# Kernel tuning notes

Measured on AMD Instinct MI355X. Metric: run time of the kernel, lower is better.

The kernel has to match this reference:

```python
import jax, jax.numpy as jnp
import numpy as np

B = 256      # number of graphs (args.batch_size)
NPG = 1000   # nodes per graph (args.num_node)
C = 64       # in_channels
DEG = 16     # avg degree
K = 500      # ceil(ratio * NPG), ratio = 0.5
EPS = 1e-8


def setup_inputs() -> dict:
    key = jax.random.key(0)
    k1, k2, k3, k4, k5 = jax.random.split(key, 5)
    N = B * NPG
    epg = NPG * DEG  # edges per graph
    x = jax.random.normal(k1, (N, C), jnp.float32)
    src = jax.random.randint(k2, (B, epg), 0, NPG)
    dst = jax.random.randint(k3, (B, epg), 0, NPG)
    off = (jnp.arange(B, dtype=jnp.int32) * NPG)[:, None]
    edge_index = jnp.stack([(src + off).reshape(-1), (dst + off).reshape(-1)]).astype(jnp.int32)
    edge_attr = jax.random.uniform(k4, (B * epg,), jnp.float32)
    batch = jnp.repeat(jnp.arange(B, dtype=jnp.int32), NPG)
    W = jax.random.normal(k5, (C, C), jnp.float32) * (1.0 / np.sqrt(C))
    b = jnp.zeros((C,), jnp.float32)
    return {"istraining": 1, "x": x, "edge_index": edge_index, "edge_attr": edge_attr,
            "batch": batch, "W": W, "b": b}


def _gcn_conv(x, edge_index, W, b):
    # PyG GCNConv: x' = D^{-1/2} (A + I) D^{-1/2} X W + b, unit edge weights.
    N = x.shape[0]
    sl = jnp.arange(N, dtype=edge_index.dtype)
    src = jnp.concatenate([edge_index[0], sl])  # message source j
    dst = jnp.concatenate([edge_index[1], sl])  # aggregation target i
    deg = jnp.zeros((N,), x.dtype).at[dst].add(1.0)
    dinv = jnp.where(deg > 0, jax.lax.rsqrt(jnp.maximum(deg, 1.0)), 0.0)
    norm = dinv[src] * dinv[dst]          # [E+N]
    h = x @ W                              # [N, C]
    msg = h[src] * norm[:, None]           # gather + scale (dominant traffic)
    out = jax.ops.segment_sum(msg, dst, num_segments=N) + b
    return out


def _node_score(x):
    # compute_node_score: cosine similarity of each node to its graph centroid
    # (community prototype), plus KL(softmax(score) || uniform) per graph.
    xb = x.reshape(B, NPG, C)
    cen = xb.mean(axis=1, keepdims=True)                       # [B,1,C]
    num = jnp.sum(xb * cen, axis=-1)                           # [B,NPG]
    den = jnp.linalg.norm(xb, axis=-1) * jnp.linalg.norm(cen, axis=-1) + EPS
    score = num / den                                          # [B,NPG]
    logp = jax.nn.log_softmax(score, axis=1)
    kl = jnp.sum(jnp.exp(logp) * (logp + jnp.log(jnp.float32(NPG))), axis=1)  # [B]
    indices_ = jnp.argsort(-score, axis=1)                     # [B,NPG]
    return score, kl, indices_


def reference(istraining, x, edge_index, edge_attr, batch, W, b):
    N = x.shape[0]
    x = _gcn_conv(x, edge_index, W, b)
    score, kl_all_batch, indices_ = _node_score(x)
    # per-graph top-k (fixed k since every graph has NPG nodes)
    _, idx = jax.lax.top_k(score, K)                           # [B,K]
    perm = ((jnp.arange(B, dtype=idx.dtype) * NPG)[:, None] + idx).reshape(-1)  # [B*K]
    score_flat = score.reshape(-1)
    x_new = x[perm] * jnp.tanh(score_flat[perm])[:, None]
    batch_new = batch[perm]
    # filter_adj: keep edges with both endpoints retained, re-index to new ids.
    mapping = jnp.full((N,), -1, dtype=jnp.int32).at[perm].set(
        jnp.arange(perm.shape[0], dtype=jnp.int32))
    new_ei = mapping[edge_index]                               # [2,E], -1 = dropped
    edge_mask = jnp.logical_and(new_ei[0] >= 0, new_ei[1] >= 0)
    edge_attr_new = jnp.where(edge_mask, edge_attr, 0.0)
    return (x_new, new_ei, edge_attr_new, edge_mask, batch_new, perm, kl_all_batch, indices_)
```

## Files before the change

kernel.cpp:

```cpp
#include <hip/hip_runtime.h>
#include <math.h>

#define NPG 1000
#define KTOP 500
#define C 64
#define EPG 16000
#define BPG 63

__device__ __forceinline__ float readlane_f(float v, int l) {
    return __uint_as_float(__builtin_amdgcn_readlane(__float_as_uint(v), (unsigned)l));
}
__device__ __forceinline__ int readlane_i(int v, int l) {
    return (int)__builtin_amdgcn_readlane((unsigned)v, (unsigned)l);
}

__global__ __launch_bounds__(1024) void build_graph_k(const int* __restrict__ ei, int E,
                                                      int* __restrict__ deg,
                                                      float* __restrict__ dinv,
                                                      int* __restrict__ off,
                                                      int* __restrict__ csr) {
    int g = blockIdx.x, t = threadIdx.x;
    __shared__ int cnt[NPG];
    __shared__ int soff[NPG];
    __shared__ unsigned short lcsr[EPG];
    __shared__ int red[1024];
    const int gbase = g * NPG;
    const int ebase = g * EPG;
    const int* __restrict__ srcp = ei + ebase;
    const int* __restrict__ dstp = ei + E + ebase;

    for (int i = t; i < NPG; i += 1024) cnt[i] = 0;
    __syncthreads();
    for (int i = t; i < EPG; i += 1024) atomicAdd(&cnt[dstp[i] - gbase], 1);
    __syncthreads();
    int v = (t < NPG) ? cnt[t] : 0;
    red[t] = v;
    __syncthreads();
    for (int o = 1; o < 1024; o <<= 1) {
        int xx = (t >= o) ? red[t - o] : 0;
        __syncthreads();
        red[t] += xx;
        __syncthreads();
    }
    if (t < NPG) soff[t] = red[t] - v;
    __syncthreads();
    for (int i = t; i < NPG; i += 1024) {
        int d = cnt[i];
        deg[gbase + i] = d;
        dinv[gbase + i] = 1.0f / sqrtf((float)(d + 1));
        off[gbase + i] = ebase + soff[i];
    }
    __syncthreads();
    for (int i = t; i < NPG; i += 1024) cnt[i] = soff[i];
    __syncthreads();
    for (int i = t; i < EPG; i += 1024) {
        int d = dstp[i] - gbase;
        int pos = atomicAdd(&cnt[d], 1);
        lcsr[pos] = (unsigned short)(srcp[i] - gbase);
    }
    __syncthreads();
    int4* co = (int4*)(csr + ebase);
    for (int i = t; i < EPG / 4; i += 1024) {
        int4 vv;
        vv.x = gbase + (int)lcsr[i * 4 + 0];
        vv.y = gbase + (int)lcsr[i * 4 + 1];
        vv.z = gbase + (int)lcsr[i * 4 + 2];
        vv.w = gbase + (int)lcsr[i * 4 + 3];
        co[i] = vv;
    }
}

__global__ __launch_bounds__(256) void gemm_k(const float* __restrict__ x,
                                              const float* __restrict__ W,
                                              const float* __restrict__ dinv,
                                              float* __restrict__ h2, int N) {
    __shared__ float sW[C * C];
    int t = threadIdx.x;
    for (int i = t; i < C * C / 4; i += 256) ((float4*)sW)[i] = ((const float4*)W)[i];
    __syncthreads();
    int r0 = blockIdx.x * 512 + t;
    int r1 = r0 + 256;
    if (r0 >= N) return;
    bool has1 = (r1 < N);
    const float4* x0 = (const float4*)(x + (size_t)r0 * C);
    const float4* x1 = (const float4*)(x + (size_t)(has1 ? r1 : r0) * C);
    float acc0[C], acc1[C];
#pragma unroll
    for (int i = 0; i < C; ++i) { acc0[i] = 0.f; acc1[i] = 0.f; }
    float4 a0 = x0[0], a1 = x1[0];
    for (int k4 = 0; k4 < 16; ++k4) {
        float4 b0, b1;
        if (k4 < 15) { b0 = x0[k4 + 1]; b1 = x1[k4 + 1]; }
        const float4* wr = (const float4*)(sW + k4 * 4 * C);
        const float* a0f = (const float*)&a0;
        const float* a1f = (const float*)&a1;
#pragma unroll
        for (int c4 = 0; c4 < 16; ++c4) {
            float4 w[4];
            w[0] = wr[c4]; w[1] = wr[16 + c4]; w[2] = wr[32 + c4]; w[3] = wr[48 + c4];
            const float* wf = (const float*)w;
#pragma unroll
            for (int j = 0; j < 4; ++j) {
                float s0 = acc0[c4 * 4 + j], s1 = acc1[c4 * 4 + j];
#pragma unroll
                for (int kk = 0; kk < 4; ++kk) {
                    float wv = wf[kk * 4 + j];
                    s0 = fmaf(a0f[kk], wv, s0);
                    s1 = fmaf(a1f[kk], wv, s1);
                }
                acc0[c4 * 4 + j] = s0; acc1[c4 * 4 + j] = s1;
            }
        }
        a0 = b0; a1 = b1;
    }
    float dv0 = dinv[r0];
    float dv1 = has1 ? dinv[r1] : 0.f;
#pragma unroll
    for (int i = 0; i < C; ++i) { acc0[i] *= dv0; acc1[i] *= dv1; }
    float4* h0 = (float4*)(h2 + (size_t)r0 * C);
#pragma unroll
    for (int q = 0; q < 16; ++q) h0[q] = ((float4*)acc0)[q];
    if (has1) {
        float4* h1 = (float4*)(h2 + (size_t)r1 * C);
#pragma unroll
        for (int q = 0; q < 16; ++q) h1[q] = ((float4*)acc1)[q];
    }
}

__global__ __launch_bounds__(256) void gather_k(const int* __restrict__ csr,
                                                const int* __restrict__ off,
                                                const int* __restrict__ deg,
                                                const float* __restrict__ h2,
                                                const float* __restrict__ dinv,
                                                const float* __restrict__ bias,
                                                float* __restrict__ out2,
                                                float* __restrict__ cen_sum,
                                                int N, int B) {
    __shared__ float cenacc[C];
    int blk = blockIdx.x;
    int wave = threadIdx.x >> 6;
    int lane = threadIdx.x & 63;
    int t = threadIdx.x;
    int g, blkin;
    if ((B & 7) == 0) {
        int xcd = blk & 7, slot = blk >> 3;
        g = (slot / BPG) * 8 + xcd;
        blkin = slot % BPG;
    } else {
        g = blk / BPG;
        blkin = blk % BPG;
    }
    if (t < C) cenacc[t] = 0.f;
    __syncthreads();

    int base = blkin * 4 + wave;
    bool active = (base < NPG / 4);
    float csum = 0.f;
    if (active) {
        int nA = g * NPG + base;
        int nB = nA + 250, nC = nA + 500, nD = nA + 750;
        int oA = off[nA], oB = off[nB], oC = off[nC], oD = off[nD];
        int dA = deg[nA], dB = deg[nB], dC = deg[nC], dD = deg[nD];
        float diA = dinv[nA], diB = dinv[nB], diC = dinv[nC], diD = dinv[nD];
        float hA = h2[(size_t)nA * C + lane];
        float hB = h2[(size_t)nB * C + lane];
        float hC = h2[(size_t)nC * C + lane];
        float hD = h2[(size_t)nD * C + lane];
        float bv = bias[lane];
        int svA = (lane < dA) ? csr[oA + lane] : nA;
        int svB = (lane < dB) ? csr[oB + lane] : nB;
        int svC = (lane < dC) ? csr[oC + lane] : nC;
        int svD = (lane < dD) ? csr[oD + lane] : nD;
        int jmA = dA < 64 ? dA : 64;
        int jmB = dB < 64 ? dB : 64;
        int jmC = dC < 64 ? dC : 64;
        int jmD = dD < 64 ? dD : 64;
        int rA = (jmA + 3) & ~3, rB = (jmB + 3) & ~3;
        int rC = (jmC + 3) & ~3, rD = (jmD + 3) & ~3;
        int m0 = rA > rB ? rA : rB;
        int m1 = rC > rD ? rC : rD;
        int mmax = m0 > m1 ? m0 : m1;
        float aA = 0.f, aB = 0.f, aC = 0.f, aD = 0.f;
        for (int j = 0; j < mmax; j += 4) {
            int sA0 = readlane_i(svA, j + 0), sA1 = readlane_i(svA, j + 1);
            int sA2 = readlane_i(svA, j + 2), sA3 = readlane_i(svA, j + 3);
            int sB0 = readlane_i(svB, j + 0), sB1 = readlane_i(svB, j + 1);
            int sB2 = readlane_i(svB, j + 2), sB3 = readlane_i(svB, j + 3);
            int sC0 = readlane_i(svC, j + 0), sC1 = readlane_i(svC, j + 1);
            int sC2 = readlane_i(svC, j + 2), sC3 = readlane_i(svC, j + 3);
            int sD0 = readlane_i(svD, j + 0), sD1 = readlane_i(svD, j + 1);
            int sD2 = readlane_i(svD, j + 2), sD3 = readlane_i(svD, j + 3);
            float vA0 = h2[(size_t)sA0 * C + lane];
            float vA1 = h2[(size_t)sA1 * C + lane];
            float vA2 = h2[(size_t)sA2 * C + lane];
            float vA3 = h2[(size_t)sA3 * C + lane];
            float vB0 = h2[(size_t)sB0 * C + lane];
            float vB1 = h2[(size_t)sB1 * C + lane];
            float vB2 = h2[(size_t)sB2 * C + lane];
            float vB3 = h2[(size_t)sB3 * C + lane];
            float vC0 = h2[(size_t)sC0 * C + lane];
            float vC1 = h2[(size_t)sC1 * C + lane];
            float vC2 = h2[(size_t)sC2 * C + lane];
            float vC3 = h2[(size_t)sC3 * C + lane];
            float vD0 = h2[(size_t)sD0 * C + lane];
            float vD1 = h2[(size_t)sD1 * C + lane];
            float vD2 = h2[(size_t)sD2 * C + lane];
            float vD3 = h2[(size_t)sD3 * C + lane];
            aA += (vA0 + vA1) + (vA2 + vA3);
            aB += (vB0 + vB1) + (vB2 + vB3);
            aC += (vC0 + vC1) + (vC2 + vC3);
            aD += (vD0 + vD1) + (vD2 + vD3);
        }
        for (int j = 64; j < dA; ++j) aA += h2[(size_t)csr[oA + j] * C + lane];
        for (int j = 64; j < dB; ++j) aB += h2[(size_t)csr[oB + j] * C + lane];
        for (int j = 64; j < dC; ++j) aC += h2[(size_t)csr[oC + j] * C + lane];
        for (int j = 64; j < dD; ++j) aD += h2[(size_t)csr[oD + j] * C + lane];
        float cA = 1.0f - (float)(mmax - jmA);
        float cB = 1.0f - (float)(mmax - jmB);
        float cC = 1.0f - (float)(mmax - jmC);
        float cD = 1.0f - (float)(mmax - jmD);
        float resA = fmaf(diA, fmaf(cA, hA, aA), bv);
        float resB = fmaf(diB, fmaf(cB, hB, aB), bv);
        float resC = fmaf(diC, fmaf(cC, hC, aC), bv);
        float resD = fmaf(diD, fmaf(cD, hD, aD), bv);
        out2[(size_t)nA * C + lane] = resA;
        out2[(size_t)nB * C + lane] = resB;
        out2[(size_t)nC * C + lane] = resC;
        out2[(size_t)nD * C + lane] = resD;
        csum = (resA + resB) + (resC + resD);
        atomicAdd(&cenacc[lane], csum);
    }
    __syncthreads();
    if (t < C) atomicAdd(&cen_sum[(size_t)g * C + t], cenacc[t]);
}

__global__ void cen_fin_k(const float* __restrict__ cen_sum, float* __restrict__ cen,
                          float* __restrict__ cnorm) {
    int g = blockIdx.x, c = threadIdx.x;
    float m = cen_sum[(size_t)g * C + c] / 1000.0f;
    cen[g * C + c] = m;
    float v = m * m;
    for (int o = 32; o > 0; o >>= 1) v += __shfl_down(v, o, 64);
    if (c == 0) cnorm[g] = sqrtf(v);
}

__global__ void score_k(const float* __restrict__ out2, const float* __restrict__ cen,
                        const float* __restrict__ cnorm, float* __restrict__ score, int N) {
    int i = blockIdx.x * 256 + threadIdx.x;
    if (i < N) {
        int g = i / NPG;
        const float4* xr = (const float4*)(out2 + (size_t)i * C);
        const float4* cr = (const float4*)(cen + g * C);
        float num = 0.f, sq = 0.f;
#pragma unroll
        for (int q = 0; q < 16; ++q) {
            float4 a = xr[q], b = cr[q];
            num += a.x * b.x + a.y * b.y + a.z * b.z + a.w * b.w;
            sq  += a.x * a.x + a.y * a.y + a.z * a.z + a.w * a.w;
        }
        float den = sqrtf(sq) * cnorm[g] + 1e-8f;
        score[i] = num / den;
    }
}

__global__ void softmax_kl_k(const float* __restrict__ score, float* __restrict__ o_kl) {
    int g = blockIdx.x, t = threadIdx.x;
    __shared__ float ss[NPG];
    __shared__ float red[256];
    const float4* s4 = (const float4*)(score + (size_t)g * NPG);
    for (int i = t; i < NPG / 4; i += 256) ((float4*)ss)[i] = s4[i];
    __syncthreads();
    float mx = -INFINITY;
    for (int i = t; i < NPG; i += 256) mx = fmaxf(mx, ss[i]);
    red[t] = mx;
    __syncthreads();
    for (int w = 128; w > 0; w >>= 1) { if (t < w) red[t] = fmaxf(red[t], red[t + w]); __syncthreads(); }
    mx = red[0];
    __syncthreads();
    float se = 0.f;
    for (int i = t; i < NPG; i += 256) se += expf(ss[i] - mx);
    red[t] = se;
    __syncthreads();
    for (int w = 128; w > 0; w >>= 1) { if (t < w) red[t] += red[t + w]; __syncthreads(); }
    float lse = logf(red[0]);
    __syncthreads();
    float kl = 0.f;
    const float ln_npg = 6.9077552790f;
    for (int i = t; i < NPG; i += 256) {
        float lp = ss[i] - mx - lse;
        kl += expf(lp) * (lp + ln_npg);
    }
    red[t] = kl;
    __syncthreads();
    for (int w = 128; w > 0; w >>= 1) { if (t < w) red[t] += red[t + w]; __syncthreads(); }
    if (t == 0) o_kl[g] = red[0];
}

__global__ __launch_bounds__(1024) void sort_k(const float* __restrict__ score,
                                               int* __restrict__ sidx,
                                               float* __restrict__ o_ind) {
    __shared__ unsigned long long kk[1024];
    int g = blockIdx.x, t = threadIdx.x;
    unsigned long long v;
    if (t < NPG) {
        unsigned u = __float_as_uint(score[(size_t)g * NPG + t]);
        u = (u & 0x80000000u) ? ~u : (u | 0x80000000u);
        v = ((unsigned long long)(~u) << 32) | (unsigned)t;
    } else {
        v = ~0ULL;
    }
    kk[t] = v;
    __syncthreads();
    for (int k = 2; k <= 1024; k <<= 1) {
        for (int j = k >> 1; j > 0; j >>= 1) {
            int ixj = t ^ j;
            if (ixj > t) {
                unsigned long long a = kk[t], b = kk[ixj];
                bool up = ((t & k) == 0);
                if ((a > b) == up) { kk[t] = b; kk[ixj] = a; }
            }
            __syncthreads();
        }
    }
    if (t < NPG) {
        int idx = (int)(kk[t] & 0xFFFFFFFFULL);
        sidx[(size_t)g * NPG + t] = idx;
        o_ind[(size_t)g * NPG + t] = (float)idx;
    }
}

__global__ void topk_k(const int* __restrict__ sidx, const float* __restrict__ score,
                       const float* __restrict__ out2, int* __restrict__ mapping,
                       float* __restrict__ o_xnew, float* __restrict__ o_batch,
                       float* __restrict__ o_perm, int BK) {
    int j = blockIdx.x * 256 + threadIdx.x;
    if (j < BK) {
        int b = j / KTOP, r = j - b * KTOP;
        int node = sidx[(size_t)b * NPG + r];
        int gn = b * NPG + node;
        mapping[gn] = j;
        o_perm[j] = (float)gn;
        o_batch[j] = (float)b;
        float tn = tanhf(score[gn]);
        const float4* src = (const float4*)(out2 + (size_t)gn * C);
        float4* dst = (float4*)(o_xnew + (size_t)j * C);
#pragma unroll
        for (int q = 0; q < 16; ++q) {
            float4 v = src[q];
            v.x *= tn; v.y *= tn; v.z *= tn; v.w *= tn;
            dst[q] = v;
        }
    }
}

__global__ void edge_out_k(const int* __restrict__ ei, const float* __restrict__ eattr,
                           const int* __restrict__ mapping, float* __restrict__ o_newei,
                           float* __restrict__ o_eattr, float* __restrict__ o_mask, int E) {
    int e4 = blockIdx.x * 256 + threadIdx.x;
    int q = E >> 2;
    if (e4 < q) {
        int4 sidx = ((const int4*)ei)[e4];
        int4 didx = ((const int4*)ei)[q + e4];
        int a0 = mapping[sidx.x], a1 = mapping[sidx.y], a2 = mapping[sidx.z], a3 = mapping[sidx.w];
        int b0 = mapping[didx.x], b1 = mapping[didx.y], b2 = mapping[didx.z], b3 = mapping[didx.w];
        float4 f0 = { (float)a0, (float)a1, (float)a2, (float)a3 };
        float4 f1 = { (float)b0, (float)b1, (float)b2, (float)b3 };
        ((float4*)o_newei)[e4] = f0;
        ((float4*)o_newei)[q + e4] = f1;
        float4 at = ((const float4*)eattr)[e4];
        float4 mk, ea;
        mk.x = (a0 >= 0 && b0 >= 0) ? 1.0f : 0.0f;
        mk.y = (a1 >= 0 && b1 >= 0) ? 1.0f : 0.0f;
        mk.z = (a2 >= 0 && b2 >= 0) ? 1.0f : 0.0f;
        mk.w = (a3 >= 0 && b3 >= 0) ? 1.0f : 0.0f;
        ea.x = mk.x != 0.0f ? at.x : 0.0f;
        ea.y = mk.y != 0.0f ? at.y : 0.0f;
        ea.z = mk.z != 0.0f ? at.z : 0.0f;
        ea.w = mk.w != 0.0f ? at.w : 0.0f;
        ((float4*)o_mask)[e4] = mk;
        ((float4*)o_eattr)[e4] = ea;
    }
}

extern "C" void kernel_launch(void* const* d_in, const int* in_sizes, int n_in,
                              void* d_out, int out_size, void* d_ws, size_t ws_size,
                              hipStream_t stream) {
    (void)n_in; (void)out_size; (void)ws_size;
    const float* x     = (const float*)d_in[1];
    const int*   ei    = (const int*)d_in[2];
    const float* eattr = (const float*)d_in[3];
    const float* W     = (const float*)d_in[5];
    const float* bias  = (const float*)d_in[6];

    const int N  = in_sizes[1] / C;
    const int E  = in_sizes[2] / 2;
    const int B  = N / NPG;
    const int BK = B * KTOP;

    char* wsp = (char*)d_ws;
    float* out2    = (float*)wsp; wsp += (size_t)N * C * 4;
    float* dinv    = (float*)wsp; wsp += (size_t)N * 4;
    float* score   = (float*)wsp; wsp += (size_t)N * 4;
    float* cen     = (float*)wsp; wsp += (size_t)B * C * 4;
    float* cnorm   = (float*)wsp; wsp += 1024;
    int*   sidx    = (int*)wsp;   wsp += (size_t)B * NPG * 4;
    int*   mapping = (int*)wsp;   wsp += (size_t)N * 4;
    int*   deg     = (int*)wsp;   wsp += (size_t)N * 4;
    int*   off     = (int*)wsp;   wsp += (size_t)N * 4;
    float* cen_sum = (float*)wsp; wsp += (size_t)B * C * 4;

    float* out     = (float*)d_out;
    float* o_xnew  = out;
    float* o_newei = o_xnew + (size_t)BK * C;
    float* o_eattr = o_newei + 2 * (size_t)E;
    float* o_mask  = o_eattr + (size_t)E;
    float* o_batch = o_mask + (size_t)E;
    float* o_perm  = o_batch + (size_t)BK;
    float* o_kl    = o_perm + (size_t)BK;
    float* o_ind   = o_kl + (size_t)B;

    float* h2buf = out;
    int*   csr   = (int*)o_eattr;

    hipMemsetAsync(mapping, 0xFF, (size_t)N * 4, stream);
    hipMemsetAsync(cen_sum, 0, (size_t)B * C * 4, stream);

    build_graph_k<<<B, 1024, 0, stream>>>(ei, E, deg, dinv, off, csr);
    gemm_k<<<(N + 511) / 512, 256, 0, stream>>>(x, W, dinv, h2buf, N);
    gather_k<<<B * BPG, 256, 0, stream>>>(csr, off, deg, h2buf, dinv, bias, out2,
                                          cen_sum, N, B);
    cen_fin_k<<<B, 64, 0, stream>>>(cen_sum, cen, cnorm);
    score_k<<<(N + 255) / 256, 256, 0, stream>>>(out2, cen, cnorm, score, N);
    softmax_kl_k<<<B, 256, 0, stream>>>(score, o_kl);
    sort_k<<<B, 1024, 0, stream>>>(score, sidx, o_ind);
    topk_k<<<(BK + 255) / 256, 256, 0, stream>>>(sidx, score, out2, mapping,
                                                 o_xnew, o_batch, o_perm, BK);
    edge_out_k<<<(E / 4 + 255) / 256, 256, 0, stream>>>(ei, eattr, mapping,
                                                        o_newei, o_eattr, o_mask, E);
}
```

Before: 397.9 us.

## Fuse per-graph score, softmax-KL, sort, top-k and edge filtering into one kernel

Result: no change. 401.2 us (+0.8%).

```diff
diff --git a/kernel.cpp b/kernel.cpp
--- a/kernel.cpp
+++ b/kernel.cpp
@@ -155,7 +155,6 @@
 
     int base = blkin * 4 + wave;
     bool active = (base < NPG / 4);
-    float csum = 0.f;
     if (active) {
         int nA = g * NPG + base;
         int nB = nA + 250, nC = nA + 500, nD = nA + 750;
@@ -182,43 +181,51 @@
         int mmax = m0 > m1 ? m0 : m1;
         float aA = 0.f, aB = 0.f, aC = 0.f, aD = 0.f;
         for (int j = 0; j < mmax; j += 4) {
-            int sA0 = readlane_i(svA, j + 0), sA1 = readlane_i(svA, j + 1);
-            int sA2 = readlane_i(svA, j + 2), sA3 = readlane_i(svA, j + 3);
-            int sB0 = readlane_i(svB, j + 0), sB1 = readlane_i(svB, j + 1);
-            int sB2 = readlane_i(svB, j + 2), sB3 = readlane_i(svB, j + 3);
-            int sC0 = readlane_i(svC, j + 0), sC1 = readlane_i(svC, j + 1);
-            int sC2 = readlane_i(svC, j + 2), sC3 = readlane_i(svC, j + 3);
-            int sD0 = readlane_i(svD, j + 0), sD1 = readlane_i(svD, j + 1);
-            int sD2 = readlane_i(svD, j + 2), sD3 = readlane_i(svD, j + 3);
-            float vA0 = h2[(size_t)sA0 * C + lane];
-            float vA1 = h2[(size_t)sA1 * C + lane];
-            float vA2 = h2[(size_t)sA2 * C + lane];
-            float vA3 = h2[(size_t)sA3 * C + lane];
-            float vB0 = h2[(size_t)sB0 * C + lane];
-            float vB1 = h2[(size_t)sB1 * C + lane];
-            float vB2 = h2[(size_t)sB2 * C + lane];
-            float vB3 = h2[(size_t)sB3 * C + lane];
-            float vC0 = h2[(size_t)sC0 * C + lane];
-            float vC1 = h2[(size_t)sC1 * C + lane];
-            float vC2 = h2[(size_t)sC2 * C + lane];
-            float vC3 = h2[(size_t)sC3 * C + lane];
-            float vD0 = h2[(size_t)sD0 * C + lane];
-            float vD1 = h2[(size_t)sD1 * C + lane];
-            float vD2 = h2[(size_t)sD2 * C + lane];
-            float vD3 = h2[(size_t)sD3 * C + lane];
-            aA += (vA0 + vA1) + (vA2 + vA3);
-            aB += (vB0 + vB1) + (vB2 + vB3);
-            aC += (vC0 + vC1) + (vC2 + vC3);
-            aD += (vD0 + vD1) + (vD2 + vD3);
+            if (j < rA) {
+                int s0 = readlane_i(svA, j + 0), s1 = readlane_i(svA, j + 1);
+                int s2 = readlane_i(svA, j + 2), s3 = readlane_i(svA, j + 3);
+                float v0 = h2[(size_t)s0 * C + lane];
+                float v1 = h2[(size_t)s1 * C + lane];
+                float v2 = h2[(size_t)s2 * C + lane];
+                float v3 = h2[(size_t)s3 * C + lane];
+                aA += (v0 + v1) + (v2 + v3);
+            }
+            if (j < rB) {
+                int s0 = readlane_i(svB, j + 0), s1 = readlane_i(svB, j + 1);
+                int s2 = readlane_i(svB, j + 2), s3 = readlane_i(svB, j + 3);
+                float v0 = h2[(size_t)s0 * C + lane];
+                float v1 = h2[(size_t)s1 * C + lane];
+                float v2 = h2[(size_t)s2 * C + lane];
+                float v3 = h2[(size_t)s3 * C + lane];
+                aB += (v0 + v1) + (v2 + v3);
+            }
+            if (j < rC) {
+                int s0 = readlane_i(svC, j + 0), s1 = readlane_i(svC, j + 1);
+                int s2 = readlane_i(svC, j + 2), s3 = readlane_i(svC, j + 3);
+                float v0 = h2[(size_t)s0 * C + lane];
+                float v1 = h2[(size_t)s1 * C + lane];
+                float v2 = h2[(size_t)s2 * C + lane];
+                float v3 = h2[(size_t)s3 * C + lane];
+                aC += (v0 + v1) + (v2 + v3);
+            }
+            if (j < rD) {
+                int s0 = readlane_i(svD, j + 0), s1 = readlane_i(svD, j + 1);
+                int s2 = readlane_i(svD, j + 2), s3 = readlane_i(svD, j + 3);
+                float v0 = h2[(size_t)s0 * C + lane];
+                float v1 = h2[(size_t)s1 * C + lane];
+                float v2 = h2[(size_t)s2 * C + lane];
+                float v3 = h2[(size_t)s3 * C + lane];
+                aD += (v0 + v1) + (v2 + v3);
+            }
         }
         for (int j = 64; j < dA; ++j) aA += h2[(size_t)csr[oA + j] * C + lane];
         for (int j = 64; j < dB; ++j) aB += h2[(size_t)csr[oB + j] * C + lane];
         for (int j = 64; j < dC; ++j) aC += h2[(size_t)csr[oC + j] * C + lane];
         for (int j = 64; j < dD; ++j) aD += h2[(size_t)csr[oD + j] * C + lane];
-        float cA = 1.0f - (float)(mmax - jmA);
-        float cB = 1.0f - (float)(mmax - jmB);
-        float cC = 1.0f - (float)(mmax - jmC);
-        float cD = 1.0f - (float)(mmax - jmD);
+        float cA = 1.0f - (float)(rA - jmA);
+        float cB = 1.0f - (float)(rB - jmB);
+        float cC = 1.0f - (float)(rC - jmC);
+        float cD = 1.0f - (float)(rD - jmD);
         float resA = fmaf(diA, fmaf(cA, hA, aA), bv);
         float resB = fmaf(diB, fmaf(cB, hB, aB), bv);
         float resC = fmaf(diC, fmaf(cC, hC, aC), bv);
@@ -227,147 +234,142 @@
         out2[(size_t)nB * C + lane] = resB;
         out2[(size_t)nC * C + lane] = resC;
         out2[(size_t)nD * C + lane] = resD;
-        csum = (resA + resB) + (resC + resD);
+        float csum = (resA + resB) + (resC + resD);
         atomicAdd(&cenacc[lane], csum);
     }
     __syncthreads();
     if (t < C) atomicAdd(&cen_sum[(size_t)g * C + t], cenacc[t]);
 }
 
-__global__ void cen_fin_k(const float* __restrict__ cen_sum, float* __restrict__ cen,
-                          float* __restrict__ cnorm) {
-    int g = blockIdx.x, c = threadIdx.x;
-    float m = cen_sum[(size_t)g * C + c] / 1000.0f;
-    cen[g * C + c] = m;
-    float v = m * m;
-    for (int o = 32; o > 0; o >>= 1) v += __shfl_down(v, o, 64);
-    if (c == 0) cnorm[g] = sqrtf(v);
-}
-
-__global__ void score_k(const float* __restrict__ out2, const float* __restrict__ cen,
-                        const float* __restrict__ cnorm, float* __restrict__ score, int N) {
-    int i = blockIdx.x * 256 + threadIdx.x;
-    if (i < N) {
-        int g = i / NPG;
-        const float4* xr = (const float4*)(out2 + (size_t)i * C);
-        const float4* cr = (const float4*)(cen + g * C);
-        float num = 0.f, sq = 0.f;
-#pragma unroll
-        for (int q = 0; q < 16; ++q) {
-            float4 a = xr[q], b = cr[q];
-            num += a.x * b.x + a.y * b.y + a.z * b.z + a.w * b.w;
-            sq  += a.x * a.x + a.y * a.y + a.z * a.z + a.w * a.w;
+__global__ __launch_bounds__(1024) void post_k(const float* __restrict__ out2,
+                                               const float* __restrict__ cen_sum,
+                                               const int* __restrict__ ei,
+                                               const float* __restrict__ eattr,
+                                               float* __restrict__ o_xnew,
+                                               float* __restrict__ o_newei,
+                                               float* __restrict__ o_eattr,
+                                               float* __restrict__ o_mask,
+                                               float* __restrict__ o_batch,
+                                               float* __restrict__ o_perm,
+                                               float* __restrict__ o_kl,
+                                               float* __restrict__ o_ind,
+                                               int E) {
+    __shared__ float ss[NPG];
+    __shared__ float red[1024];
+    __shared__ unsigned long long kk[1024];
+    __shared__ int   map[NPG];
+    __shared__ float cenl[C];
+    __shared__ float cns;
+    int g = blockIdx.x, t = threadIdx.x;
+    int wave = t >> 6, lane = t & 63;
+    const int gbase = g * NPG;
+    const int ebase = g * EPG;
+
+    if (t < C) cenl[t] = cen_sum[(size_t)g * C + t] * (1.0f / 1000.0f);
+    __syncthreads();
+    if (t < 64) {
+        float m = cenl[t];
+        float v = m * m;
+        for (int o = 32; o > 0; o >>= 1) v += __shfl_down(v, o, 64);
+        if (t == 0) cns = sqrtf(v);
+    }
+    __syncthreads();
+    float cv = cenl[lane];
+    float cn = cns;
+    for (int n = wave; n < NPG; n += 16) {
+        float a = out2[(size_t)(gbase + n) * C + lane];
+        float num = a * cv;
+        float sq = a * a;
+        for (int o = 32; o > 0; o >>= 1) {
+            num += __shfl_down(num, o, 64);
+            sq  += __shfl_down(sq, o, 64);
         }
-        float den = sqrtf(sq) * cnorm[g] + 1e-8f;
-        score[i] = num / den;
-    }
-}
-
-__global__ void softmax_kl_k(const float* __restrict__ score, float* __restrict__ o_kl) {
-    int g = blockIdx.x, t = threadIdx.x;
-    __shared__ float ss[NPG];
-    __shared__ float red[256];
-    const float4* s4 = (const float4*)(score + (size_t)g * NPG);
-    for (int i = t; i < NPG / 4; i += 256) ((float4*)ss)[i] = s4[i];
+        if (lane == 0) ss[n] = num / (sqrtf(sq) * cn + 1e-8f);
+    }
     __syncthreads();
     float mx = -INFINITY;
-    for (int i = t; i < NPG; i += 256) mx = fmaxf(mx, ss[i]);
+    for (int i = t; i < NPG; i += 1024) mx = fmaxf(mx, ss[i]);
     red[t] = mx;
     __syncthreads();
-    for (int w = 128; w > 0; w >>= 1) { if (t < w) red[t] = fmaxf(red[t], red[t + w]); __syncthreads(); }
+    for (int w = 512; w > 0; w >>= 1) { if (t < w) red[t] = fmaxf(red[t], red[t + w]); __syncthreads(); }
     mx = red[0];
     __syncthreads();
     float se = 0.f;
-    for (int i = t; i < NPG; i += 256) se += expf(ss[i] - mx);
+    for (int i = t; i < NPG; i += 1024) se += expf(ss[i] - mx);
     red[t] = se;
     __syncthreads();
-    for (int w = 128; w > 0; w >>= 1) { if (t < w) red[t] += red[t + w]; __syncthreads(); }
+    for (int w = 512; w > 0; w >>= 1) { if (t < w) red[t] += red[t + w]; __syncthreads(); }
     float lse = logf(red[0]);
     __syncthreads();
     float kl = 0.f;
     const float ln_npg = 6.9077552790f;
-    for (int i = t; i < NPG; i += 256) {
+    for (int i = t; i < NPG; i += 1024) {
         float lp = ss[i] - mx - lse;
         kl += expf(lp) * (lp + ln_npg);
     }
     red[t] = kl;
     __syncthreads();
-    for (int w = 128; w > 0; w >>= 1) { if (t < w) red[t] += red[t + w]; __syncthreads(); }
+    for (int w = 512; w > 0; w >>= 1) { if (t < w) red[t] += red[t + w]; __syncthreads(); }
     if (t == 0) o_kl[g] = red[0];
-}
-
-__global__ __launch_bounds__(1024) void sort_k(const float* __restrict__ score,
-                                               int* __restrict__ sidx,
-                                               float* __restrict__ o_ind) {
-    __shared__ unsigned long long kk[1024];
-    int g = blockIdx.x, t = threadIdx.x;
     unsigned long long v;
     if (t < NPG) {
-        unsigned u = __float_as_uint(score[(size_t)g * NPG + t]);
+        unsigned u = __float_as_uint(ss[t]);
         u = (u & 0x80000000u) ? ~u : (u | 0x80000000u);
         v = ((unsigned long long)(~u) << 32) | (unsigned)t;
     } else {
         v = ~0ULL;
     }
+    __syncthreads();
     kk[t] = v;
     __syncthreads();
     for (int k = 2; k <= 1024; k <<= 1) {
         for (int j = k >> 1; j > 0; j >>= 1) {
             int ixj = t ^ j;
             if (ixj > t) {
-                unsigned long long a = kk[t], b = kk[ixj];
+                unsigned long long a = kk[t], b2 = kk[ixj];
                 bool up = ((t & k) == 0);
-                if ((a > b) == up) { kk[t] = b; kk[ixj] = a; }
+                if ((a > b2) == up) { kk[t] = b2; kk[ixj] = a; }
             }
             __syncthreads();
         }
     }
     if (t < NPG) {
         int idx = (int)(kk[t] & 0xFFFFFFFFULL);
-        sidx[(size_t)g * NPG + t] = idx;
         o_ind[(size_t)g * NPG + t] = (float)idx;
-    }
-}
-
-__global__ void topk_k(const int* __restrict__ sidx, const float* __restrict__ score,
-                       const float* __restrict__ out2, int* __restrict__ mapping,
-                       float* __restrict__ o_xnew, float* __restrict__ o_batch,
-                       float* __restrict__ o_perm, int BK) {
-    int j = blockIdx.x * 256 + threadIdx.x;
-    if (j < BK) {
-        int b = j / KTOP, r = j - b * KTOP;
-        int node = sidx[(size_t)b * NPG + r];
-        int gn = b * NPG + node;
-        mapping[gn] = j;
-        o_perm[j] = (float)gn;
-        o_batch[j] = (float)b;
-        float tn = tanhf(score[gn]);
-        const float4* src = (const float4*)(out2 + (size_t)gn * C);
-        float4* dst = (float4*)(o_xnew + (size_t)j * C);
-#pragma unroll
-        for (int q = 0; q < 16; ++q) {
-            float4 v = src[q];
-            v.x *= tn; v.y *= tn; v.z *= tn; v.w *= tn;
-            dst[q] = v;
-        }
-    }
-}
-
-__global__ void edge_out_k(const int* __restrict__ ei, const float* __restrict__ eattr,
-                           const int* __restrict__ mapping, float* __restrict__ o_newei,
-                           float* __restrict__ o_eattr, float* __restrict__ o_mask, int E) {
-    int e4 = blockIdx.x * 256 + threadIdx.x;
-    int q = E >> 2;
-    if (e4 < q) {
-        int4 sidx = ((const int4*)ei)[e4];
-        int4 didx = ((const int4*)ei)[q + e4];
-        int a0 = mapping[sidx.x], a1 = mapping[sidx.y], a2 = mapping[sidx.z], a3 = mapping[sidx.w];
-        int b0 = mapping[didx.x], b1 = mapping[didx.y], b2 = mapping[didx.z], b3 = mapping[didx.w];
+        map[t] = -1;
+    }
+    __syncthreads();
+    if (t < KTOP) {
+        int node = (int)(kk[t] & 0xFFFFFFFFULL);
+        map[node] = g * KTOP + t;
+        o_perm[(size_t)g * KTOP + t] = (float)(gbase + node);
+        o_batch[(size_t)g * KTOP + t] = (float)g;
+    }
+    __syncthreads();
+    for (int r = wave; r < KTOP; r += 16) {
+        int node = (int)(kk[r] & 0xFFFFFFFFULL);
+        float tn = tanhf(ss[node]);
+        o_xnew[((size_t)g * KTOP + r) * C + lane] =
+            out2[(size_t)(gbase + node) * C + lane] * tn;
+    }
+    const int4* src4 = (const int4*)(ei + ebase);
+    const int4* dst4 = (const int4*)(ei + E + ebase);
+    const float4* at4 = (const float4*)(eattr + ebase);
+    float4* nei0 = (float4*)(o_newei + ebase);
+    float4* nei1 = (float4*)(o_newei + E + ebase);
+    float4* msk4 = (float4*)(o_mask + ebase);
+    float4* eat4 = (float4*)(o_eattr + ebase);
+    for (int e4 = t; e4 < EPG / 4; e4 += 1024) {
+        int4 s = src4[e4], d = dst4[e4];
+        int a0 = map[s.x - gbase], a1 = map[s.y - gbase];
+        int a2 = map[s.z - gbase], a3 = map[s.w - gbase];
+        int b0 = map[d.x - gbase], b1 = map[d.y - gbase];
+        int b2 = map[d.z - gbase], b3 = map[d.w - gbase];
         float4 f0 = { (float)a0, (float)a1, (float)a2, (float)a3 };
         float4 f1 = { (float)b0, (float)b1, (float)b2, (float)b3 };
-        ((float4*)o_newei)[e4] = f0;
-        ((float4*)o_newei)[q + e4] = f1;
-        float4 at = ((const float4*)eattr)[e4];
+        nei0[e4] = f0;
+        nei1[e4] = f1;
+        float4 at = at4[e4];
         float4 mk, ea;
         mk.x = (a0 >= 0 && b0 >= 0) ? 1.0f : 0.0f;
         mk.y = (a1 >= 0 && b1 >= 0) ? 1.0f : 0.0f;
@@ -377,8 +379,8 @@
         ea.y = mk.y != 0.0f ? at.y : 0.0f;
         ea.z = mk.z != 0.0f ? at.z : 0.0f;
         ea.w = mk.w != 0.0f ? at.w : 0.0f;
-        ((float4*)o_mask)[e4] = mk;
-        ((float4*)o_eattr)[e4] = ea;
+        msk4[e4] = mk;
+        eat4[e4] = ea;
     }
 }
 
@@ -400,11 +402,6 @@
     char* wsp = (char*)d_ws;
     float* out2    = (float*)wsp; wsp += (size_t)N * C * 4;
     float* dinv    = (float*)wsp; wsp += (size_t)N * 4;
-    float* score   = (float*)wsp; wsp += (size_t)N * 4;
-    float* cen     = (float*)wsp; wsp += (size_t)B * C * 4;
-    float* cnorm   = (float*)wsp; wsp += 1024;
-    int*   sidx    = (int*)wsp;   wsp += (size_t)B * NPG * 4;
-    int*   mapping = (int*)wsp;   wsp += (size_t)N * 4;
     int*   deg     = (int*)wsp;   wsp += (size_t)N * 4;
     int*   off     = (int*)wsp;   wsp += (size_t)N * 4;
     float* cen_sum = (float*)wsp; wsp += (size_t)B * C * 4;
@@ -422,19 +419,13 @@
     float* h2buf = out;
     int*   csr   = (int*)o_eattr;
 
-    hipMemsetAsync(mapping, 0xFF, (size_t)N * 4, stream);
     hipMemsetAsync(cen_sum, 0, (size_t)B * C * 4, stream);
 
     build_graph_k<<<B, 1024, 0, stream>>>(ei, E, deg, dinv, off, csr);
     gemm_k<<<(N + 511) / 512, 256, 0, stream>>>(x, W, dinv, h2buf, N);
     gather_k<<<B * BPG, 256, 0, stream>>>(csr, off, deg, h2buf, dinv, bias, out2,
                                           cen_sum, N, B);
-    cen_fin_k<<<B, 64, 0, stream>>>(cen_sum, cen, cnorm);
-    score_k<<<(N + 255) / 256, 256, 0, stream>>>(out2, cen, cnorm, score, N);
-    softmax_kl_k<<<B, 256, 0, stream>>>(score, o_kl);
-    sort_k<<<B, 1024, 0, stream>>>(score, sidx, o_ind);
-    topk_k<<<(BK + 255) / 256, 256, 0, stream>>>(sidx, score, out2, mapping,
-                                                 o_xnew, o_batch, o_perm, BK);
-    edge_out_k<<<(E / 4 + 255) / 256, 256, 0, stream>>>(ei, eattr, mapping,
-                                                        o_newei, o_eattr, o_mask, E);
-}
+    post_k<<<B, 1024, 0, stream>>>(out2, cen_sum, ei, eattr,
+                                   o_xnew, o_newei, o_eattr, o_mask,
+                                   o_batch, o_perm, o_kl, o_ind, E);
+}
```
